# Kernel optimization log

Hardware: AMD Instinct MI355X
Metric: run time of the kernel (lower is better)

Reference implementation:

```python
import jax, jax.numpy as jnp
import numpy as np

B, D, S = 8192, 1024, 32  # batch, feature dim, number of sessions (experts)


def setup_inputs() -> dict:
    key = jax.random.key(0)
    k1, k2, k3, k4 = jax.random.split(key, 4)
    x = jax.random.normal(k1, (B, D), dtype=jnp.float32)
    # Expert bank: original init is identity affine; perturb so the test is nontrivial.
    W = jnp.eye(D, dtype=jnp.float32)[None, :, :] + 0.02 * jax.random.normal(k2, (S, D, D), dtype=jnp.float32)
    b = 0.02 * jax.random.normal(k3, (S, D), dtype=jnp.float32)
    session_idx = jax.random.randint(k4, (B,), 0, S)  # int session id per sample
    return {"x": x, "W": W, "b": b, "session_idx": session_idx}


def reference(x, W, b, session_idx):
    """Per-sample session-affine dispatch: out[i] = W[session_idx[i]] @ x[i] + b[session_idx[i]].

    Implemented as a scan over the (small, fixed) set of S experts: one dense
    [B,D]x[D,D] GEMM per expert, masked-accumulated into the output. This avoids
    gathering a [B,D,D] per-sample weight tensor.
    """
    num_sessions = W.shape[0]

    def step(acc, packed):
        Ws, bs, s = packed                       # Ws: [D,D], bs: [D]
        y = x @ Ws.T + bs                        # [B,D] dense affine for expert s
        mask = (session_idx == s)[:, None]       # [B,1] samples belonging to s
        return acc + jnp.where(mask, y, jnp.zeros((), x.dtype)), None

    out, _ = jax.lax.scan(step, jnp.zeros_like(x), (W, b, jnp.arange(num_sessions)))
    return out
```

## Files before the change

kernel.cpp:

```cpp
#include <hip/hip_runtime.h>
#include <cstddef>

#define B_ROWS 8192
#define DIM    1024
#define NSESS  32
#define MT     256
#define NTILE  256
#define BK     32
#define KITERS (DIM / BK)
#define TPE    2
#define LROW   40
#define TSZ    (MT * LROW)
#define NXCD   8
#define EPX    (NSESS / NXCD)
#define BPE    (TPE * (DIM / NTILE))

typedef __attribute__((ext_vector_type(8))) short short8;
typedef __attribute__((ext_vector_type(4))) float floatx4;
typedef __attribute__((ext_vector_type(4))) int intx4;
typedef __attribute__((ext_vector_type(2))) unsigned int uintx2;

__device__ __forceinline__ unsigned pack_bf16_2(float fa, float fb) {
  unsigned a = __builtin_bit_cast(unsigned, fa);
  unsigned b = __builtin_bit_cast(unsigned, fb);
  a += 0x7fffu + ((a >> 16) & 1u);
  b += 0x7fffu + ((b >> 16) & 1u);
  return __builtin_amdgcn_perm(b, a, 0x07060302u);
}

__global__ __launch_bounds__(512, 2) void gemm_kernel(
    const float* __restrict__ x, const float* __restrict__ W,
    const float* __restrict__ bias, const int* __restrict__ sidx,
    float* __restrict__ out)
{
  __shared__ __align__(16) short lds[4 * TSZ];
  __shared__ int row_ids[MT];
  __shared__ int psum[512];
  short* const As0 = lds;
  short* const Bs0 = lds + TSZ;
  short* const As1 = lds + 2 * TSZ;
  short* const Bs1 = lds + 3 * TSZ;

  const int hw    = blockIdx.x;
  const int xcd   = hw & (NXCD - 1);
  const int r     = hw >> 3;
  const int s     = xcd * EPX + (r / BPE);
  const int rr    = r % BPE;
  const int ntile = rr >> 1;
  const int mtile = rr & 1;
  const int tid   = threadIdx.x;

  const int lane = tid & 63;
  const int wv   = tid >> 6;
  const int wm   = wv >> 2;
  const int wn   = wv & 3;
  const int fr   = lane & 15;
  const int kg   = lane >> 4;

  const int srw = tid >> 3;
  const int sch = tid & 7;

  unsigned boff[4];
  floatx4 wr0[4], wr1[4];
  {
    const unsigned wbyte =
        (unsigned)(((size_t)s * DIM * DIM + (size_t)(ntile * NTILE) * DIM) * 4u);
#pragma unroll
    for (int j = 0; j < 4; ++j) {
      const int tr = j * 64 + srw;
      boff[j] = wbyte + (unsigned)((tr * DIM + sch * 4) * 4);
      wr0[j] = *(const floatx4*)((const char*)W + boff[j]);
    }
#pragma unroll
    for (int j = 0; j < 4; ++j)
      wr1[j] = *(const floatx4*)((const char*)W + boff[j] + (BK * 4));
  }

  const intx4* sv = (const intx4*)(sidx + tid * 16);
  int c = 0;
#pragma unroll
  for (int j = 0; j < 4; ++j) {
    const intx4 v = sv[j];
#pragma unroll
    for (int e = 0; e < 4; ++e) c += (v[e] == s);
  }
  psum[tid] = c;
  __syncthreads();
#pragma unroll
  for (int d = 1; d < 512; d <<= 1) {
    const int mine = psum[tid];
    const int add  = (tid >= d) ? psum[tid - d] : 0;
    __syncthreads();
    psum[tid] = mine + add;
    __syncthreads();
  }
  const int total = psum[511];
  const int h     = (total + 1) >> 1;
  const int lo    = mtile * h;
  const int hi    = mtile ? total : h;
  const int nrows = hi - lo;
  if (nrows == 0) return;
  const int base_rank = psum[tid] - c;

  if (tid < MT) row_ids[tid] = -1;
  __syncthreads();
  {
    int r2 = base_rank;
#pragma unroll
    for (int j = 0; j < 4; ++j) {
      const intx4 v = sv[j];
#pragma unroll
      for (int e = 0; e < 4; ++e) {
        if (v[e] == s) {
          if (r2 >= lo && r2 < hi) row_ids[r2 - lo] = tid * 16 + 4 * j + e;
          ++r2;
        }
      }
    }
  }
  __syncthreads();

  unsigned aoff[4];
  floatx4 xr0[4], xr1[4];
#pragma unroll
  for (int j = 0; j < 4; ++j) {
    int ar = row_ids[j * 64 + srw];
    if (ar < 0) ar = 0;
    aoff[j] = (unsigned)((ar * DIM + sch * 4) * 4);
    xr0[j] = *(const floatx4*)((const char*)x + aoff[j]);
  }
#pragma unroll
  for (int j = 0; j < 4; ++j)
    xr1[j] = *(const floatx4*)((const char*)x + aoff[j] + (BK * 4));

  floatx4 acc[8][4] = {};

#define LOADSET(XR, WR, KB)                                                    \
  {                                                                            \
    _Pragma("unroll")                                                          \
    for (int j = 0; j < 4; ++j)                                                \
      XR[j] = *(const floatx4*)((const char*)x + aoff[j] + (KB) * (BK * 4));   \
    _Pragma("unroll")                                                          \
    for (int j = 0; j < 4; ++j)                                                \
      WR[j] = *(const floatx4*)((const char*)W + boff[j] + (KB) * (BK * 4));   \
  }

#define CVTWRITE(XR, WR, AS, BS)                                               \
  {                                                                            \
    _Pragma("unroll")                                                          \
    for (int j = 0; j < 4; ++j) {                                              \
      const int off = (j * 64 + srw) * LROW + sch * 4;                         \
      uintx2 ua = { pack_bf16_2(XR[j][0], XR[j][1]),                           \
                    pack_bf16_2(XR[j][2], XR[j][3]) };                         \
      uintx2 ub = { pack_bf16_2(WR[j][0], WR[j][1]),                           \
                    pack_bf16_2(WR[j][2], WR[j][3]) };                         \
      *(uintx2*)&AS[off] = ua;                                                 \
      *(uintx2*)&BS[off] = ub;                                                 \
    }                                                                          \
  }

#define COMPUTE(AS, BS)                                                        \
  {                                                                            \
    short8 fb[4];                                                              \
    _Pragma("unroll")                                                          \
    for (int i = 0; i < 4; ++i)                                                \
      fb[i] = *(const short8*)&BS[(wn * 64 + i * 16 + fr) * LROW + kg * 8];    \
    _Pragma("unroll")                                                          \
    for (int mi = 0; mi < 8; ++mi) {                                           \
      const short8 fa = *(const short8*)&AS[(wm * 128 + mi * 16 + fr) * LROW + kg * 8]; \
      _Pragma("unroll")                                                        \
      for (int ni = 0; ni < 4; ++ni)                                           \
        acc[mi][ni] = __builtin_amdgcn_mfma_f32_16x16x32_bf16(                 \
            fa, fb[ni], acc[mi][ni], 0, 0, 0);                                 \
    }                                                                          \
  }

  CVTWRITE(xr0, wr0, As0, Bs0);
  __syncthreads();

  for (int kb = 0; kb < KITERS; kb += 2) {
    if (kb + 2 < KITERS) LOADSET(xr0, wr0, kb + 2);
    COMPUTE(As0, Bs0);
    CVTWRITE(xr1, wr1, As1, Bs1);
    __syncthreads();

    if (kb + 3 < KITERS) LOADSET(xr1, wr1, kb + 3);
    COMPUTE(As1, Bs1);
    if (kb + 2 < KITERS) CVTWRITE(xr0, wr0, As0, Bs0);
    __syncthreads();
  }

#undef LOADSET
#undef CVTWRITE
#undef COMPUTE

  __syncthreads();
  float* obuf = (float*)lds;
  const int col0 = ntile * NTILE + wn * 64;
  float bv[4];
#pragma unroll
  for (int ni = 0; ni < 4; ++ni) bv[ni] = bias[s * DIM + col0 + ni * 16 + fr];

  const int rbase = tid >> 6;
  const int ch    = tid & 63;

#pragma unroll
  for (int p = 0; p < 8; ++p) {
    if (p * 32 >= nrows) break;
    if (wm == (p >> 2)) {
#pragma unroll
      for (int mh = 0; mh < 2; ++mh) {
        const int mi = (p & 3) * 2 + mh;
        const int lr = mi * 16 + kg * 4 - (p & 3) * 32;
#pragma unroll
        for (int q = 0; q < 4; ++q)
#pragma unroll
          for (int ni = 0; ni < 4; ++ni)
            obuf[(lr + q) * 260 + wn * 64 + ni * 16 + fr] = acc[mi][ni][q] + bv[ni];
      }
    }
    __syncthreads();
#pragma unroll
    for (int j = 0; j < 4; ++j) {
      const int lr = j * 8 + rbase;
      const int ml = p * 32 + lr;
      if (ml < nrows) {
        const int orow = row_ids[ml];
        const floatx4 v = *(const floatx4*)&obuf[lr * 260 + ch * 4];
        *(floatx4*)&out[(size_t)orow * DIM + ntile * NTILE + ch * 4] = v;
      }
    }
    __syncthreads();
  }
}

extern "C" void kernel_launch(void* const* d_in, const int* in_sizes, int n_in,
                              void* d_out, int out_size, void* d_ws, size_t ws_size,
                              hipStream_t stream) {
  const float* x    = (const float*)d_in[0];
  const float* W    = (const float*)d_in[1];
  const float* b    = (const float*)d_in[2];
  const int*   sidx = (const int*)d_in[3];
  float* out = (float*)d_out;
  (void)d_ws; (void)ws_size;

  hipLaunchKernelGGL(gemm_kernel, dim3(NSESS * TPE * (DIM / NTILE)), dim3(512),
                     0, stream, x, W, b, sidx, out);
}
```

Baseline: 245.2 us.

## Shrink M tile to 192 rows, deepen register prefetch, use wave-shuffle scan

Cuts the per-block row tile from 256 to 192, since each half-expert block holds only about 128 gathered rows. This removes MFMA work and LDS traffic spent on padded rows. It also replaces the LDS prefix-sum with a wave-level shuffle scan plus a cross-wave sum, and moves to a three-deep register prefetch with a fully unrolled K loop. The risk is that a half-session holding more than 192 rows would overflow the tile, and the third register buffer raises register pressure.

```diff
diff --git a/kernel.cpp b/kernel.cpp
--- a/kernel.cpp
+++ b/kernel.cpp
@@ -4,13 +4,14 @@
 #define B_ROWS 8192
 #define DIM    1024
 #define NSESS  32
-#define MT     256
+#define MT     192
 #define NTILE  256
 #define BK     32
 #define KITERS (DIM / BK)
 #define TPE    2
 #define LROW   40
-#define TSZ    (MT * LROW)
+#define TSZA   (MT * LROW)
+#define TSZB   (NTILE * LROW)
 #define NXCD   8
 #define EPX    (NSESS / NXCD)
 #define BPE    (TPE * (DIM / NTILE))
@@ -33,13 +34,13 @@
     const float* __restrict__ bias, const int* __restrict__ sidx,
     float* __restrict__ out)
 {
-  __shared__ __align__(16) short lds[4 * TSZ];
+  __shared__ __align__(16) short lds[2 * TSZA + 2 * TSZB];
   __shared__ int row_ids[MT];
-  __shared__ int psum[512];
+  __shared__ int wsum[8];
   short* const As0 = lds;
-  short* const Bs0 = lds + TSZ;
-  short* const As1 = lds + 2 * TSZ;
-  short* const Bs1 = lds + 3 * TSZ;
+  short* const As1 = lds + TSZA;
+  short* const Bs0 = lds + 2 * TSZA;
+  short* const Bs1 = lds + 2 * TSZA + TSZB;
 
   const int hw    = blockIdx.x;
   const int xcd   = hw & (NXCD - 1);
@@ -61,7 +62,7 @@
   const int sch = tid & 7;
 
   unsigned boff[4];
-  floatx4 wr0[4], wr1[4];
+  floatx4 wr0[4], wr1[4], wr2[4];
   {
     const unsigned wbyte =
         (unsigned)(((size_t)s * DIM * DIM + (size_t)(ntile * NTILE) * DIM) * 4u);
@@ -74,6 +75,9 @@
 #pragma unroll
     for (int j = 0; j < 4; ++j)
       wr1[j] = *(const floatx4*)((const char*)W + boff[j] + (BK * 4));
+#pragma unroll
+    for (int j = 0; j < 4; ++j)
+      wr2[j] = *(const floatx4*)((const char*)W + boff[j] + 2 * (BK * 4));
   }
 
   const intx4* sv = (const intx4*)(sidx + tid * 16);
@@ -84,23 +88,27 @@
 #pragma unroll
     for (int e = 0; e < 4; ++e) c += (v[e] == s);
   }
-  psum[tid] = c;
-  __syncthreads();
-#pragma unroll
-  for (int d = 1; d < 512; d <<= 1) {
-    const int mine = psum[tid];
-    const int add  = (tid >= d) ? psum[tid - d] : 0;
-    __syncthreads();
-    psum[tid] = mine + add;
-    __syncthreads();
-  }
-  const int total = psum[511];
+  int ic = c;
+#pragma unroll
+  for (int d = 1; d < 64; d <<= 1) {
+    const int t = __shfl_up(ic, d);
+    if (lane >= d) ic += t;
+  }
+  if (lane == 63) wsum[wv] = ic;
+  __syncthreads();
+  int wbase = 0, total = 0;
+#pragma unroll
+  for (int w = 0; w < 8; ++w) {
+    const int v = wsum[w];
+    total += v;
+    if (w < wv) wbase += v;
+  }
   const int h     = (total + 1) >> 1;
   const int lo    = mtile * h;
   const int hi    = mtile ? total : h;
   const int nrows = hi - lo;
   if (nrows == 0) return;
-  const int base_rank = psum[tid] - c;
+  const int base_rank = wbase + ic - c;
 
   if (tid < MT) row_ids[tid] = -1;
   __syncthreads();
@@ -120,25 +128,28 @@
   }
   __syncthreads();
 
-  unsigned aoff[4];
-  floatx4 xr0[4], xr1[4];
-#pragma unroll
-  for (int j = 0; j < 4; ++j) {
+  unsigned aoff[3];
+  floatx4 xr0[3], xr1[3], xr2[3];
+#pragma unroll
+  for (int j = 0; j < 3; ++j) {
     int ar = row_ids[j * 64 + srw];
     if (ar < 0) ar = 0;
     aoff[j] = (unsigned)((ar * DIM + sch * 4) * 4);
     xr0[j] = *(const floatx4*)((const char*)x + aoff[j]);
   }
 #pragma unroll
-  for (int j = 0; j < 4; ++j)
+  for (int j = 0; j < 3; ++j)
     xr1[j] = *(const floatx4*)((const char*)x + aoff[j] + (BK * 4));
-
-  floatx4 acc[8][4] = {};
+#pragma unroll
+  for (int j = 0; j < 3; ++j)
+    xr2[j] = *(const floatx4*)((const char*)x + aoff[j] + 2 * (BK * 4));
+
+  floatx4 acc[6][4] = {};
 
 #define LOADSET(XR, WR, KB)                                                    \
   {                                                                            \
     _Pragma("unroll")                                                          \
-    for (int j = 0; j < 4; ++j)                                                \
+    for (int j = 0; j < 3; ++j)                                                \
       XR[j] = *(const floatx4*)((const char*)x + aoff[j] + (KB) * (BK * 4));   \
     _Pragma("unroll")                                                          \
     for (int j = 0; j < 4; ++j)                                                \
@@ -148,13 +159,17 @@
 #define CVTWRITE(XR, WR, AS, BS)                                               \
   {                                                                            \
     _Pragma("unroll")                                                          \
-    for (int j = 0; j < 4; ++j) {                                              \
+    for (int j = 0; j < 3; ++j) {                                              \
       const int off = (j * 64 + srw) * LROW + sch * 4;                         \
       uintx2 ua = { pack_bf16_2(XR[j][0], XR[j][1]),                           \
                     pack_bf16_2(XR[j][2], XR[j][3]) };                         \
+      *(uintx2*)&AS[off] = ua;                                                 \
+    }                                                                          \
+    _Pragma("unroll")                                                          \
+    for (int j = 0; j < 4; ++j) {                                              \
+      const int off = (j * 64 + srw) * LROW + sch * 4;                         \
       uintx2 ub = { pack_bf16_2(WR[j][0], WR[j][1]),                           \
                     pack_bf16_2(WR[j][2], WR[j][3]) };                         \
-      *(uintx2*)&AS[off] = ua;                                                 \
       *(uintx2*)&BS[off] = ub;                                                 \
     }                                                                          \
   }
@@ -166,8 +181,8 @@
     for (int i = 0; i < 4; ++i)                                                \
       fb[i] = *(const short8*)&BS[(wn * 64 + i * 16 + fr) * LROW + kg * 8];    \
     _Pragma("unroll")                                                          \
-    for (int mi = 0; mi < 8; ++mi) {                                           \
-      const short8 fa = *(const short8*)&AS[(wm * 128 + mi * 16 + fr) * LROW + kg * 8]; \
+    for (int mi = 0; mi < 6; ++mi) {                                           \
+      const short8 fa = *(const short8*)&AS[(wm * 96 + mi * 16 + fr) * LROW + kg * 8]; \
       _Pragma("unroll")                                                        \
       for (int ni = 0; ni < 4; ++ni)                                           \
         acc[mi][ni] = __builtin_amdgcn_mfma_f32_16x16x32_bf16(                 \
@@ -175,26 +190,35 @@
     }                                                                          \
   }
 
+#define PHASE(K, CUR, NXT, XR, WR)                                             \
+  {                                                                            \
+    COMPUTE(As##CUR, Bs##CUR);                                                 \
+    if ((K) + 1 < KITERS) CVTWRITE(XR, WR, As##NXT, Bs##NXT);                  \
+    if ((K) + 4 < KITERS) LOADSET(XR, WR, (K) + 4);                            \
+    __syncthreads();                                                           \
+  }
+
   CVTWRITE(xr0, wr0, As0, Bs0);
-  __syncthreads();
-
-  for (int kb = 0; kb < KITERS; kb += 2) {
-    if (kb + 2 < KITERS) LOADSET(xr0, wr0, kb + 2);
-    COMPUTE(As0, Bs0);
-    CVTWRITE(xr1, wr1, As1, Bs1);
-    __syncthreads();
-
-    if (kb + 3 < KITERS) LOADSET(xr1, wr1, kb + 3);
-    COMPUTE(As1, Bs1);
-    if (kb + 2 < KITERS) CVTWRITE(xr0, wr0, As0, Bs0);
-    __syncthreads();
-  }
-
+  LOADSET(xr0, wr0, 3);
+  __syncthreads();
+
+  PHASE( 0, 0, 1, xr1, wr1)  PHASE( 1, 1, 0, xr2, wr2)  PHASE( 2, 0, 1, xr0, wr0)
+  PHASE( 3, 1, 0, xr1, wr1)  PHASE( 4, 0, 1, xr2, wr2)  PHASE( 5, 1, 0, xr0, wr0)
+  PHASE( 6, 0, 1, xr1, wr1)  PHASE( 7, 1, 0, xr2, wr2)  PHASE( 8, 0, 1, xr0, wr0)
+  PHASE( 9, 1, 0, xr1, wr1)  PHASE(10, 0, 1, xr2, wr2)  PHASE(11, 1, 0, xr0, wr0)
+  PHASE(12, 0, 1, xr1, wr1)  PHASE(13, 1, 0, xr2, wr2)  PHASE(14, 0, 1, xr0, wr0)
+  PHASE(15, 1, 0, xr1, wr1)  PHASE(16, 0, 1, xr2, wr2)  PHASE(17, 1, 0, xr0, wr0)
+  PHASE(18, 0, 1, xr1, wr1)  PHASE(19, 1, 0, xr2, wr2)  PHASE(20, 0, 1, xr0, wr0)
+  PHASE(21, 1, 0, xr1, wr1)  PHASE(22, 0, 1, xr2, wr2)  PHASE(23, 1, 0, xr0, wr0)
+  PHASE(24, 0, 1, xr1, wr1)  PHASE(25, 1, 0, xr2, wr2)  PHASE(26, 0, 1, xr0, wr0)
+  PHASE(27, 1, 0, xr1, wr1)  PHASE(28, 0, 1, xr2, wr2)  PHASE(29, 1, 0, xr0, wr0)
+  PHASE(30, 0, 1, xr1, wr1)  PHASE(31, 1, 0, xr2, wr2)
+
+#undef PHASE
 #undef LOADSET
 #undef CVTWRITE
 #undef COMPUTE
 
-  __syncthreads();
   float* obuf = (float*)lds;
   const int col0 = ntile * NTILE + wn * 64;
   float bv[4];
@@ -205,13 +229,13 @@
   const int ch    = tid & 63;
 
 #pragma unroll
-  for (int p = 0; p < 8; ++p) {
+  for (int p = 0; p < 6; ++p) {
     if (p * 32 >= nrows) break;
-    if (wm == (p >> 2)) {
+    if (wm == (p >= 3 ? 1 : 0)) {
 #pragma unroll
       for (int mh = 0; mh < 2; ++mh) {
-        const int mi = (p & 3) * 2 + mh;
-        const int lr = mi * 16 + kg * 4 - (p & 3) * 32;
+        const int mi = (p % 3) * 2 + mh;
+        const int lr = mi * 16 + kg * 4 - (p % 3) * 32;
 #pragma unroll
         for (int q = 0; q < 4; ++q)
 #pragma unroll
```

Result: no change. 248.0 us (+1.2%).
